# Optimization experiments

Measured on AMD Instinct MI355X. Metric: run time of the kernel, lower is better.

Reference implementation:

```python
import jax, jax.numpy as jnp
import numpy as np

B, N = 32, 16
H, W = 256, 256  # image_size = (width, height) = (256, 256)
SIGMA = 0.1
RADIUS = 0.2


def _make_coord_grid():
    y = jnp.linspace(0.0, 1.0, H)  # [H]
    x = jnp.linspace(0.0, 1.0, W)  # [W]
    xg = jnp.broadcast_to(x[None, :], (H, W))
    yg = jnp.broadcast_to(y[:, None], (H, W))
    return jnp.stack([xg, yg], axis=0)  # [2, H, W], channel 0 = x, 1 = y


def setup_inputs() -> dict:
    key = jax.random.key(0)
    k1, k2, k3 = jax.random.split(key, 3)
    pred_landmarks = jax.random.uniform(k1, (B, N, 2), dtype=jnp.float32)
    target_landmarks = jax.random.uniform(k2, (B, N, 2), dtype=jnp.float32)
    visibility = jax.random.uniform(k3, (B, N), dtype=jnp.float32)
    coord_grid = _make_coord_grid().astype(jnp.float32)
    return {
        "pred_landmarks": pred_landmarks,
        "target_landmarks": target_landmarks,
        "visibility": visibility,
        "coord_grid": coord_grid,
    }


def reference(pred_landmarks, target_landmarks, visibility, coord_grid):
    # coord_grid: [2, H, W]; landmarks: [B, N, 2]
    grid = coord_grid[None, None]                      # [1, 1, 2, H, W]
    tgt = target_landmarks[..., None, None]            # [B, N, 2, 1, 1]
    prd = pred_landmarks[..., None, None]              # [B, N, 2, 1, 1]

    # Euclidean distance from every grid point to target / pred landmark.
    d_tgt = jnp.sqrt(jnp.sum((grid - tgt) ** 2, axis=2))  # [B, N, H, W]
    d_prd = jnp.sqrt(jnp.sum((grid - prd) ** 2, axis=2))  # [B, N, H, W]

    # Gaussian weights around the target, hard-masked at RADIUS.
    w = jnp.exp(-(d_tgt ** 2) / (2.0 * SIGMA ** 2))
    w = w * (d_tgt <= RADIUS).astype(w.dtype)

    num = jnp.sum(w * d_prd, axis=(-1, -2))            # [B, N]
    den = jnp.sum(w, axis=(-1, -2)) + 1e-8             # [B, N]
    per_landmark = num / den                           # [B, N]

    # Skip landmarks with visibility < 0.5 (contribute 0, like `continue`).
    vis_mask = (visibility >= 0.5).astype(per_landmark.dtype)
    total = jnp.sum(per_landmark * vis_mask)
    return total / (B * N + 1e-8)
```

## Files before the change

### kernel.cpp

```cpp
#include <hip/hip_runtime.h>


#define BB 32
#define NN 16
#define HH 256
#define WW 256
#define BN (BB * NN)

__global__ __launch_bounds__(256) void gkl_phase1(
    const float* __restrict__ pred,
    const float* __restrict__ tgt,
    const float* __restrict__ vis,
    const float* __restrict__ cg,
    float* __restrict__ ws)
{
    const int bn = blockIdx.x;
    const int t  = threadIdx.x;

    if (vis[bn] < 0.5f) { if (t == 0) ws[bn] = 0.0f; return; }

    const float tx = tgt[bn * 2 + 0], ty = tgt[bn * 2 + 1];
    const float px = pred[bn * 2 + 0], py = pred[bn * 2 + 1];

    const float R = 0.2f;
    const int j_lo = max(0,      (int)floorf((tx - R) * 255.0f) - 1);
    const int j_hi = min(WW - 1, (int)ceilf ((tx + R) * 255.0f) + 1);
    const int i_lo = max(0,      (int)floorf((ty - R) * 255.0f) - 1);
    const int i_hi = min(HH - 1, (int)ceilf ((ty + R) * 255.0f) + 1);
    const int bw = j_hi - j_lo + 1;
    const int bh = i_hi - i_lo + 1;

    __shared__ float4 colA[128];
    __shared__ float4 rowA[128];
    __shared__ float  s_n[4], s_d[4];

    if (t < 128) {
        if (t < bw) {
            const float x   = cg[j_lo + t];
            const float dxt = x - tx, dxp = x - px;
            colA[t] = make_float4(dxt * dxt, expf(-50.0f * dxt * dxt),
                                  dxp * dxp, 0.0f);
        }
    } else {
        const int r = t - 128;
        if (r < bh) {
            const float y   = cg[HH * WW + (i_lo + r) * WW];
            const float dyt = y - ty, dyp = y - py;
            rowA[r] = make_float4(dyt * dyt, expf(-50.0f * dyt * dyt),
                                  dyp * dyp, 0.0f);
        }
    }
    __syncthreads();

    const int lane = t & 63;
    const int wid  = t >> 6;

    float num = 0.0f, den = 0.0f;
    for (int r = wid; r < bh; r += 4) {
        const float4 rv = rowA[r];
        for (int c = lane; c < bw; c += 64) {
            const float4 cv = colA[c];
            const float d2t = cv.x + rv.x;
            const float dt  = sqrtf(d2t);
            float w = cv.y * rv.y;
            w = (dt <= 0.2f) ? w : 0.0f;
            const float dp = sqrtf(cv.z + rv.z);
            num = fmaf(w, dp, num);
            den += w;
        }
    }

    for (int off = 32; off > 0; off >>= 1) {
        num += __shfl_down(num, off);
        den += __shfl_down(den, off);
    }
    if (lane == 0) { s_n[wid] = num; s_d[wid] = den; }
    __syncthreads();
    if (t == 0) {
        const float n_tot = s_n[0] + s_n[1] + s_n[2] + s_n[3];
        const float d_tot = s_d[0] + s_d[1] + s_d[2] + s_d[3];
        ws[bn] = n_tot / (d_tot + 1e-8f);
    }
}

__global__ __launch_bounds__(512) void gkl_phase2(
    const float* __restrict__ ws, float* __restrict__ out)
{
    const int t = threadIdx.x;
    float v = ws[t];
    for (int off = 32; off > 0; off >>= 1) v += __shfl_down(v, off);
    __shared__ float s[8];
    if ((t & 63) == 0) s[t >> 6] = v;
    __syncthreads();
    if (t == 0) {
        float tot = 0.0f;
        #pragma unroll
        for (int i = 0; i < 8; ++i) tot += s[i];
        out[0] = tot * (1.0f / 512.0f);
    }
}

extern "C" void kernel_launch(void* const* d_in, const int* in_sizes, int n_in,
                              void* d_out, int out_size, void* d_ws, size_t ws_size,
                              hipStream_t stream) {
    const float* pred = (const float*)d_in[0];
    const float* tgt  = (const float*)d_in[1];
    const float* vis  = (const float*)d_in[2];
    const float* cg   = (const float*)d_in[3];
    float* ws  = (float*)d_ws;
    float* out = (float*)d_out;

    gkl_phase1<<<BN, 256, 0, stream>>>(pred, tgt, vis, cg, ws);
    gkl_phase2<<<1, 512, 0, stream>>>(ws, out);
}
```

Baseline: 17.96 us.

## Fuse both phases into one cooperative kernel with a grid-wide sync

```diff
diff --git a/kernel.cpp b/kernel.cpp
--- a/kernel.cpp
+++ b/kernel.cpp
@@ -1,4 +1,7 @@
 #include <hip/hip_runtime.h>
+#include <hip/hip_cooperative_groups.h>
+
+namespace cg = cooperative_groups;
 
 
 #define BB 32
@@ -6,48 +9,55 @@
 #define HH 256
 #define WW 256
 #define BN (BB * NN)
+#define NBLK 128
+#define TPB 1024
 
-__global__ __launch_bounds__(256) void gkl_phase1(
+__global__ __launch_bounds__(TPB) void gkl_fused(
     const float* __restrict__ pred,
     const float* __restrict__ tgt,
     const float* __restrict__ vis,
-    const float* __restrict__ cg,
-    float* __restrict__ ws)
+    const float* __restrict__ cgr,
+    float* __restrict__ ws,
+    float* __restrict__ out)
 {
-    const int bn = blockIdx.x;
-    const int t  = threadIdx.x;
+    const int s  = threadIdx.x >> 8;
+    const int t  = threadIdx.x & 255;
+    const int bn = (blockIdx.x << 2) + s;
 
-    if (vis[bn] < 0.5f) { if (t == 0) ws[bn] = 0.0f; return; }
+    __shared__ float4 colA[4][128];
+    __shared__ float4 rowA[4][128];
+    __shared__ float  s_n[4][4], s_d[4][4];
 
-    const float tx = tgt[bn * 2 + 0], ty = tgt[bn * 2 + 1];
-    const float px = pred[bn * 2 + 0], py = pred[bn * 2 + 1];
+    const bool visb = vis[bn] >= 0.5f;
 
-    const float R = 0.2f;
-    const int j_lo = max(0,      (int)floorf((tx - R) * 255.0f) - 1);
-    const int j_hi = min(WW - 1, (int)ceilf ((tx + R) * 255.0f) + 1);
-    const int i_lo = max(0,      (int)floorf((ty - R) * 255.0f) - 1);
-    const int i_hi = min(HH - 1, (int)ceilf ((ty + R) * 255.0f) + 1);
-    const int bw = j_hi - j_lo + 1;
-    const int bh = i_hi - i_lo + 1;
+    int i_lo = 0, bw = 0, bh = 0;
+    if (visb) {
+        const float tx = tgt[bn * 2 + 0], ty = tgt[bn * 2 + 1];
+        const float px = pred[bn * 2 + 0], py = pred[bn * 2 + 1];
 
-    __shared__ float4 colA[128];
-    __shared__ float4 rowA[128];
-    __shared__ float  s_n[4], s_d[4];
+        const float R = 0.2f;
+        const int j_lo = max(0,      (int)floorf((tx - R) * 255.0f) - 1);
+        const int j_hi = min(WW - 1, (int)ceilf ((tx + R) * 255.0f) + 1);
+        i_lo           = max(0,      (int)floorf((ty - R) * 255.0f) - 1);
+        const int i_hi = min(HH - 1, (int)ceilf ((ty + R) * 255.0f) + 1);
+        bw = j_hi - j_lo + 1;
+        bh = i_hi - i_lo + 1;
 
-    if (t < 128) {
-        if (t < bw) {
-            const float x   = cg[j_lo + t];
-            const float dxt = x - tx, dxp = x - px;
-            colA[t] = make_float4(dxt * dxt, expf(-50.0f * dxt * dxt),
-                                  dxp * dxp, 0.0f);
-        }
-    } else {
-        const int r = t - 128;
-        if (r < bh) {
-            const float y   = cg[HH * WW + (i_lo + r) * WW];
-            const float dyt = y - ty, dyp = y - py;
-            rowA[r] = make_float4(dyt * dyt, expf(-50.0f * dyt * dyt),
-                                  dyp * dyp, 0.0f);
+        if (t < 128) {
+            if (t < bw) {
+                const float x   = cgr[j_lo + t];
+                const float dxt = x - tx, dxp = x - px;
+                colA[s][t] = make_float4(dxt * dxt, expf(-50.0f * dxt * dxt),
+                                         dxp * dxp, 0.0f);
+            }
+        } else {
+            const int r = t - 128;
+            if (r < bh) {
+                const float y   = cgr[HH * WW + (i_lo + r) * WW];
+                const float dyt = y - ty, dyp = y - py;
+                rowA[s][r] = make_float4(dyt * dyt, expf(-50.0f * dyt * dyt),
+                                         dyp * dyp, 0.0f);
+            }
         }
     }
     __syncthreads();
@@ -56,47 +66,48 @@
     const int wid  = t >> 6;
 
     float num = 0.0f, den = 0.0f;
-    for (int r = wid; r < bh; r += 4) {
-        const float4 rv = rowA[r];
-        for (int c = lane; c < bw; c += 64) {
-            const float4 cv = colA[c];
-            const float d2t = cv.x + rv.x;
-            const float dt  = sqrtf(d2t);
-            float w = cv.y * rv.y;
-            w = (dt <= 0.2f) ? w : 0.0f;
-            const float dp = sqrtf(cv.z + rv.z);
-            num = fmaf(w, dp, num);
-            den += w;
+    if (visb) {
+        for (int r = wid; r < bh; r += 4) {
+            const float4 rv = rowA[s][r];
+            for (int c = lane; c < bw; c += 64) {
+                const float4 cv = colA[s][c];
+                const float d2t = cv.x + rv.x;
+                float w = cv.y * rv.y;
+                w = (sqrtf(d2t) <= 0.2f) ? w : 0.0f;
+                const float dp = sqrtf(cv.z + rv.z);
+                num = fmaf(w, dp, num);
+                den += w;
+            }
         }
     }
-
     for (int off = 32; off > 0; off >>= 1) {
         num += __shfl_down(num, off);
         den += __shfl_down(den, off);
     }
-    if (lane == 0) { s_n[wid] = num; s_d[wid] = den; }
+    if (lane == 0) { s_n[s][wid] = num; s_d[s][wid] = den; }
     __syncthreads();
     if (t == 0) {
-        const float n_tot = s_n[0] + s_n[1] + s_n[2] + s_n[3];
-        const float d_tot = s_d[0] + s_d[1] + s_d[2] + s_d[3];
-        ws[bn] = n_tot / (d_tot + 1e-8f);
+        const float nt = s_n[s][0] + s_n[s][1] + s_n[s][2] + s_n[s][3];
+        const float dt = s_d[s][0] + s_d[s][1] + s_d[s][2] + s_d[s][3];
+        ws[bn] = visb ? (nt / (dt + 1e-8f)) : 0.0f;
     }
-}
 
-__global__ __launch_bounds__(512) void gkl_phase2(
-    const float* __restrict__ ws, float* __restrict__ out)
-{
-    const int t = threadIdx.x;
-    float v = ws[t];
-    for (int off = 32; off > 0; off >>= 1) v += __shfl_down(v, off);
-    __shared__ float s[8];
-    if ((t & 63) == 0) s[t >> 6] = v;
-    __syncthreads();
-    if (t == 0) {
-        float tot = 0.0f;
-        #pragma unroll
-        for (int i = 0; i < 8; ++i) tot += s[i];
-        out[0] = tot * (1.0f / 512.0f);
+    cg::this_grid().sync();
+
+    if (blockIdx.x == 0) {
+        const int tid = threadIdx.x;
+        float v = (tid < BN) ? ws[tid] : 0.0f;
+        for (int off = 32; off > 0; off >>= 1) v += __shfl_down(v, off);
+        float* sred = &s_n[0][0];
+        __syncthreads();
+        if ((tid & 63) == 0) sred[tid >> 6] = v;
+        __syncthreads();
+        if (tid == 0) {
+            float tot = 0.0f;
+            #pragma unroll
+            for (int i = 0; i < 16; ++i) tot += sred[i];
+            out[0] = tot * (1.0f / 512.0f);
+        }
     }
 }
 
@@ -106,10 +117,12 @@
     const float* pred = (const float*)d_in[0];
     const float* tgt  = (const float*)d_in[1];
     const float* vis  = (const float*)d_in[2];
-    const float* cg   = (const float*)d_in[3];
+    const float* cgr  = (const float*)d_in[3];
     float* ws  = (float*)d_ws;
     float* out = (float*)d_out;
 
-    gkl_phase1<<<BN, 256, 0, stream>>>(pred, tgt, vis, cg, ws);
-    gkl_phase2<<<1, 512, 0, stream>>>(ws, out);
+    void* args[] = { (void*)&pred, (void*)&tgt, (void*)&vis, (void*)&cgr,
+                     (void*)&ws, (void*)&out };
+    hipLaunchCooperativeKernel((const void*)gkl_fused, dim3(NBLK), dim3(TPB),
+                               args, 0, stream);
 }
```

Result: slower. 50.80 us (+182.8%).
